# Kernel tuning notes

Hardware: AMD Instinct MI355X
Metric: run time of the kernel (lower is better)

Reference implementation:

```python
import jax, jax.numpy as jnp
import numpy as np

NODE_DIM, MSG_DIM, PROP_DIM, HIDDEN = 64, 64, 32, 128
V, T, S = 10000, 8, 16


def setup_inputs() -> dict:
    key = jax.random.key(0)
    ks = jax.random.split(key, 8)
    in_dim = NODE_DIM + MSG_DIM + 1 + PROP_DIM  # concat width of the attn MLP
    return {
        "h_t": jax.random.normal(ks[0], (V, NODE_DIM), dtype=jnp.float32),
        "messages": jax.random.normal(ks[1], (V, T, S, MSG_DIM), dtype=jnp.float32),
        "tau_values": jax.random.uniform(ks[2], (T,), dtype=jnp.float32),
        "theta": jax.random.normal(ks[3], (V, PROP_DIM), dtype=jnp.float32),
        "W1": jax.random.normal(ks[4], (in_dim, HIDDEN), dtype=jnp.float32) * 0.02,
        "b1": jnp.zeros((HIDDEN,), dtype=jnp.float32),
        "W2": jax.random.normal(ks[5], (HIDDEN, 1), dtype=jnp.float32) * 0.02,
        "b2": jnp.zeros((1,), dtype=jnp.float32),
    }


def reference(h_t, messages, tau_values, theta, W1, b1, W2, b2):
    # Equivalent to concat([h_exp, messages, tau_exp, theta_exp]) @ W1:
    # split W1 by input block and sum the partial projections, avoiding the
    # materialized (V, T, S, node+msg+1+prop) broadcast-concat tensor.
    Wh = W1[:NODE_DIM]                                  # (node_dim, H)
    Wm = W1[NODE_DIM:NODE_DIM + MSG_DIM]                # (msg_dim, H)
    Wt = W1[NODE_DIM + MSG_DIM]                         # (H,) -- the tau row
    Wp = W1[NODE_DIM + MSG_DIM + 1:]                    # (prop_dim, H)

    hidden = (
        jnp.einsum("vtsd,dh->vtsh", messages, Wm)       # (V, T, S, H)
        + (h_t @ Wh)[:, None, None, :]                  # broadcast over T, S
        + tau_values[None, :, None, None] * Wt[None, None, None, :]
        + (theta @ Wp)[:, None, None, :]
        + b1
    )
    hidden = jax.nn.relu(hidden)
    logits = (hidden @ W2 + b2)[..., 0]                 # (V, T, S)
    return logits
```

## Files before the change

### kernel.cpp

```cpp
#include <hip/hip_runtime.h>
#include <hip/hip_bf16.h>

#define VN 10000
#define HID 128

using bf16x8 = __attribute__((ext_vector_type(8))) __bf16;
using bf16x4 = __attribute__((ext_vector_type(4))) __bf16;
using f32x4  = __attribute__((ext_vector_type(4))) float;

__global__ __launch_bounds__(256) void prep_kernel(
    const float* __restrict__ h_t, const float* __restrict__ theta,
    const float* __restrict__ W1, const float* __restrict__ b1,
    float* __restrict__ base, __bf16* __restrict__ wmt)
{
  const int blk = blockIdx.x;
  const int tid = threadIdx.x;
  if (blk < 625) {
    __shared__ float in[16][96];
    const int v0 = blk * 16;
    {
      const float4* src = (const float4*)(h_t + (size_t)v0 * 64);
      float4 f = src[tid];
      int vl = tid >> 4, c = (tid & 15) * 4;
      in[vl][c] = f.x; in[vl][c + 1] = f.y; in[vl][c + 2] = f.z; in[vl][c + 3] = f.w;
    }
    if (tid < 128) {
      const float4* src = (const float4*)(theta + (size_t)v0 * 32);
      float4 f = src[tid];
      int vl = tid >> 3, c = 64 + (tid & 7) * 4;
      in[vl][c] = f.x; in[vl][c + 1] = f.y; in[vl][c + 2] = f.z; in[vl][c + 3] = f.w;
    }
    __syncthreads();
    const int h = tid & 127;
    const int half = tid >> 7;
    float acc[8];
    const float bb = b1[h];
    #pragma unroll
    for (int k = 0; k < 8; k++) acc[k] = bb;
    for (int d = 0; d < 64; d++) {
      float w = W1[d * 128 + h];
      #pragma unroll
      for (int k = 0; k < 8; k++) acc[k] += in[2 * k + half][d] * w;
    }
    for (int d = 0; d < 32; d++) {
      float w = W1[(129 + d) * 128 + h];
      #pragma unroll
      for (int k = 0; k < 8; k++) acc[k] += in[2 * k + half][64 + d] * w;
    }
    #pragma unroll
    for (int k = 0; k < 8; k++)
      base[(size_t)(v0 + 2 * k + half) * 128 + h] = acc[k];
  } else {
    int j = (blk - 625) * 256 + tid;
    int n = j >> 6, d = j & 63;
    wmt[j] = (__bf16)W1[(64 + d) * 128 + n];
  }
}

__global__ __launch_bounds__(256) void main_kernel(
    const float* __restrict__ messages, const float* __restrict__ tau,
    const float* __restrict__ W1, const float* __restrict__ W2,
    const float* __restrict__ b2, const float* __restrict__ base,
    const __bf16* __restrict__ wmt, float* __restrict__ out)
{
  __shared__ __align__(16) __bf16 lA[128 * 72];
  __shared__ __align__(16) __bf16 lB[128 * 72];
  __shared__ float lOut[128];

  const int v = blockIdx.x;
  const int tid = threadIdx.x;
  const int w = tid >> 6;
  const int lane = tid & 63;
  const int quad = lane >> 4;
  const int l16 = lane & 15;

  {
    const float4* src = (const float4*)(messages + (size_t)v * 8192);
    #pragma unroll
    for (int j = 0; j < 8; j++) {
      int idx = j * 256 + tid;
      float4 f = src[idx];
      int r = idx >> 4, c = (idx & 15) * 4;
      bf16x4 p;
      p[0] = (__bf16)f.x; p[1] = (__bf16)f.y; p[2] = (__bf16)f.z; p[3] = (__bf16)f.w;
      *(bf16x4*)&lA[r * 72 + c] = p;
    }
  }
  {
    const uint4* src = (const uint4*)wmt;
    #pragma unroll
    for (int j = 0; j < 4; j++) {
      int idx = j * 256 + tid;
      uint4 u = src[idx];
      int r = idx >> 3, c = (idx & 7) * 8;
      *(uint4*)&lB[r * 72 + c] = u;
    }
  }
  __syncthreads();

  f32x4 acc[2][8];
  #pragma unroll
  for (int mt = 0; mt < 2; mt++)
    #pragma unroll
    for (int nt = 0; nt < 8; nt++) acc[mt][nt] = (f32x4){0.f, 0.f, 0.f, 0.f};

  #pragma unroll
  for (int ks = 0; ks < 2; ks++) {
    const int k = ks * 32 + quad * 8;
    bf16x8 a[2], b[8];
    #pragma unroll
    for (int mt = 0; mt < 2; mt++) {
      int m = 32 * w + mt * 16 + l16;
      a[mt] = *(const bf16x8*)&lA[m * 72 + k];
    }
    #pragma unroll
    for (int nt = 0; nt < 8; nt++) {
      int n = nt * 16 + l16;
      b[nt] = *(const bf16x8*)&lB[n * 72 + k];
    }
    #pragma unroll
    for (int mt = 0; mt < 2; mt++)
      #pragma unroll
      for (int nt = 0; nt < 8; nt++)
        acc[mt][nt] = __builtin_amdgcn_mfma_f32_16x16x32_bf16(a[mt], b[nt], acc[mt][nt], 0, 0, 0);
  }

  float bb[8], w2[8], wt[8];
  #pragma unroll
  for (int nt = 0; nt < 8; nt++) {
    int n = nt * 16 + l16;
    bb[nt] = base[(size_t)v * 128 + n];
    w2[nt] = W2[n];
    wt[nt] = W1[128 * 128 + n];
  }
  #pragma unroll
  for (int mt = 0; mt < 2; mt++) {
    const int t = 2 * w + mt;
    const float tv = tau[t];
    float ps[4] = {0.f, 0.f, 0.f, 0.f};
    #pragma unroll
    for (int nt = 0; nt < 8; nt++) {
      const float add = bb[nt] + tv * wt[nt];
      f32x4 a4 = acc[mt][nt];
      #pragma unroll
      for (int r = 0; r < 4; r++) {
        float hdn = a4[r] + add;
        hdn = fmaxf(hdn, 0.f);
        ps[r] += hdn * w2[nt];
      }
    }
    #pragma unroll
    for (int off = 1; off < 16; off <<= 1)
      #pragma unroll
      for (int r = 0; r < 4; r++) ps[r] += __shfl_xor(ps[r], off, 64);
    if (l16 == 0) {
      #pragma unroll
      for (int r = 0; r < 4; r++)
        lOut[32 * w + mt * 16 + quad * 4 + r] = ps[r];
    }
  }
  __syncthreads();
  if (tid < 128) out[(size_t)v * 128 + tid] = lOut[tid] + b2[0];
}

extern "C" void kernel_launch(void* const* d_in, const int* in_sizes, int n_in,
                              void* d_out, int out_size, void* d_ws, size_t ws_size,
                              hipStream_t stream) {
  const float* h_t      = (const float*)d_in[0];
  const float* messages = (const float*)d_in[1];
  const float* tau      = (const float*)d_in[2];
  const float* theta    = (const float*)d_in[3];
  const float* W1       = (const float*)d_in[4];
  const float* b1       = (const float*)d_in[5];
  const float* W2       = (const float*)d_in[6];
  const float* b2       = (const float*)d_in[7];
  float* out = (float*)d_out;

  float* base = (float*)d_ws;
  __bf16* wmt = (__bf16*)((char*)d_ws + (size_t)VN * HID * sizeof(float));

  prep_kernel<<<625 + 32, 256, 0, stream>>>(h_t, theta, W1, b1, base, wmt);
  main_kernel<<<VN, 256, 0, stream>>>(messages, tau, W1, W2, b2, base, wmt, out);
}
```

Baseline: 459.2 us.

## Load MFMA operands directly from global memory into registers, dropping LDS staging

The main kernel no longer stages the message tile and the transposed W1 block through shared memory. Each lane now loads its A fragment straight from global memory as fp32, converts it to bf16 in registers, and reads its B fragments straight from the bf16 weight buffer, which removes the LDS round trip and one block barrier. Epilogue operands (base, W2, tau, b2) are loaded up front so their latency overlaps the message loads, and the launch bounds request three blocks per SM. In exchange, global reads of messages are strided per lane rather than fully coalesced, each wave re-reads the weight block from cache, and the register budget is tighter.

```diff
diff --git a/kernel.cpp b/kernel.cpp
--- a/kernel.cpp
+++ b/kernel.cpp
@@ -5,7 +5,6 @@
 #define HID 128
 
 using bf16x8 = __attribute__((ext_vector_type(8))) __bf16;
-using bf16x4 = __attribute__((ext_vector_type(4))) __bf16;
 using f32x4  = __attribute__((ext_vector_type(4))) float;
 
 __global__ __launch_bounds__(256) void prep_kernel(
@@ -37,11 +36,13 @@
     const float bb = b1[h];
     #pragma unroll
     for (int k = 0; k < 8; k++) acc[k] = bb;
+    #pragma unroll 8
     for (int d = 0; d < 64; d++) {
       float w = W1[d * 128 + h];
       #pragma unroll
       for (int k = 0; k < 8; k++) acc[k] += in[2 * k + half][d] * w;
     }
+    #pragma unroll 8
     for (int d = 0; d < 32; d++) {
       float w = W1[(129 + d) * 128 + h];
       #pragma unroll
@@ -57,14 +58,12 @@
   }
 }
 
-__global__ __launch_bounds__(256) void main_kernel(
+__global__ __launch_bounds__(256, 3) void main_kernel(
     const float* __restrict__ messages, const float* __restrict__ tau,
     const float* __restrict__ W1, const float* __restrict__ W2,
     const float* __restrict__ b2, const float* __restrict__ base,
     const __bf16* __restrict__ wmt, float* __restrict__ out)
 {
-  __shared__ __align__(16) __bf16 lA[128 * 72];
-  __shared__ __align__(16) __bf16 lB[128 * 72];
   __shared__ float lOut[128];
 
   const int v = blockIdx.x;
@@ -74,29 +73,31 @@
   const int quad = lane >> 4;
   const int l16 = lane & 15;
 
-  {
-    const float4* src = (const float4*)(messages + (size_t)v * 8192);
+  const float* msg = messages + (size_t)v * 8192;
+  float4 araw[2][2][2];
+  #pragma unroll
+  for (int mt = 0; mt < 2; mt++) {
     #pragma unroll
-    for (int j = 0; j < 8; j++) {
-      int idx = j * 256 + tid;
-      float4 f = src[idx];
-      int r = idx >> 4, c = (idx & 15) * 4;
-      bf16x4 p;
-      p[0] = (__bf16)f.x; p[1] = (__bf16)f.y; p[2] = (__bf16)f.z; p[3] = (__bf16)f.w;
-      *(bf16x4*)&lA[r * 72 + c] = p;
+    for (int ks = 0; ks < 2; ks++) {
+      const int m = 32 * w + mt * 16 + l16;
+      const float4* p = (const float4*)(msg + m * 64 + ks * 32 + quad * 8);
+      araw[mt][ks][0] = p[0];
+      araw[mt][ks][1] = p[1];
     }
   }
-  {
-    const uint4* src = (const uint4*)wmt;
-    #pragma unroll
-    for (int j = 0; j < 4; j++) {
-      int idx = j * 256 + tid;
-      uint4 u = src[idx];
-      int r = idx >> 3, c = (idx & 7) * 8;
-      *(uint4*)&lB[r * 72 + c] = u;
-    }
+
+  float bb[8], w2[8], wt[8];
+  #pragma unroll
+  for (int nt = 0; nt < 8; nt++) {
+    const int n = nt * 16 + l16;
+    bb[nt] = base[(size_t)v * 128 + n];
+    w2[nt] = W2[n];
+    wt[nt] = W1[128 * 128 + n];
   }
-  __syncthreads();
+  float tv[2];
+  tv[0] = tau[2 * w];
+  tv[1] = tau[2 * w + 1];
+  const float b2v = b2[0];
 
   f32x4 acc[2][8];
   #pragma unroll
@@ -106,46 +107,32 @@
 
   #pragma unroll
   for (int ks = 0; ks < 2; ks++) {
-    const int k = ks * 32 + quad * 8;
-    bf16x8 a[2], b[8];
+    bf16x8 b[8];
+    #pragma unroll
+    for (int nt = 0; nt < 8; nt++)
+      b[nt] = *(const bf16x8*)&wmt[(nt * 16 + l16) * 64 + ks * 32 + quad * 8];
     #pragma unroll
     for (int mt = 0; mt < 2; mt++) {
-      int m = 32 * w + mt * 16 + l16;
-      a[mt] = *(const bf16x8*)&lA[m * 72 + k];
-    }
-    #pragma unroll
-    for (int nt = 0; nt < 8; nt++) {
-      int n = nt * 16 + l16;
-      b[nt] = *(const bf16x8*)&lB[n * 72 + k];
-    }
-    #pragma unroll
-    for (int mt = 0; mt < 2; mt++)
+      const float* af = (const float*)&araw[mt][ks][0];
+      bf16x8 a;
+      #pragma unroll
+      for (int j = 0; j < 8; j++) a[j] = (__bf16)af[j];
       #pragma unroll
       for (int nt = 0; nt < 8; nt++)
-        acc[mt][nt] = __builtin_amdgcn_mfma_f32_16x16x32_bf16(a[mt], b[nt], acc[mt][nt], 0, 0, 0);
+        acc[mt][nt] = __builtin_amdgcn_mfma_f32_16x16x32_bf16(a, b[nt], acc[mt][nt], 0, 0, 0);
+    }
   }
 
-  float bb[8], w2[8], wt[8];
-  #pragma unroll
-  for (int nt = 0; nt < 8; nt++) {
-    int n = nt * 16 + l16;
-    bb[nt] = base[(size_t)v * 128 + n];
-    w2[nt] = W2[n];
-    wt[nt] = W1[128 * 128 + n];
-  }
   #pragma unroll
   for (int mt = 0; mt < 2; mt++) {
-    const int t = 2 * w + mt;
-    const float tv = tau[t];
     float ps[4] = {0.f, 0.f, 0.f, 0.f};
     #pragma unroll
     for (int nt = 0; nt < 8; nt++) {
-      const float add = bb[nt] + tv * wt[nt];
+      const float add = bb[nt] + tv[mt] * wt[nt];
       f32x4 a4 = acc[mt][nt];
       #pragma unroll
       for (int r = 0; r < 4; r++) {
-        float hdn = a4[r] + add;
-        hdn = fmaxf(hdn, 0.f);
+        float hdn = fmaxf(a4[r] + add, 0.f);
         ps[r] += hdn * w2[nt];
       }
     }
@@ -160,7 +147,7 @@
     }
   }
   __syncthreads();
-  if (tid < 128) out[(size_t)v * 128 + tid] = lOut[tid] + b2[0];
+  if (tid < 128) out[(size_t)v * 128 + tid] = lOut[tid] + b2v;
 }
 
 extern "C" void kernel_launch(void* const* d_in, const int* in_sizes, int n_in,
```

Result: slower. 472.7 us (+2.9%).
